# Optimization experiments

Hardware: AMD Instinct MI355X
Metric: run time of the kernel (lower is better)

The kernel has to match this reference:

```python
import jax, jax.numpy as jnp
import numpy as np

VOCAB, D = 100000, 128
B, V, S = 1024, 20, 30
N_CLASS = 20
H0, H1 = 256, 128  # hidden_dims


def setup_inputs() -> dict:
    key = jax.random.key(0)
    ks = jax.random.split(key, 10)
    diag_idx = jax.random.randint(ks[0], (B, V, S), 0, VOCAB, dtype=jnp.int32)
    proc_idx = jax.random.randint(ks[1], (B, V, S), 0, VOCAB, dtype=jnp.int32)
    embedding = jax.random.normal(ks[2], (VOCAB, D), dtype=jnp.float32)
    # fc0: (2D -> H0), fc1: (H0 -> H1), fc2: (H1 -> n_class); torch Linear layout [out,in]
    W0 = jax.random.normal(ks[3], (H0, 2 * D), dtype=jnp.float32) * (1.0 / np.sqrt(2 * D))
    b0 = jnp.zeros((H0,), dtype=jnp.float32)
    W1 = jax.random.normal(ks[4], (H1, H0), dtype=jnp.float32) * (1.0 / np.sqrt(H0))
    b1 = jnp.zeros((H1,), dtype=jnp.float32)
    W2 = jax.random.normal(ks[5], (N_CLASS, H1), dtype=jnp.float32) * (1.0 / np.sqrt(H1))
    b2 = jnp.zeros((N_CLASS,), dtype=jnp.float32)
    return {"diag_idx": diag_idx, "proc_idx": proc_idx, "embedding": embedding,
            "W0": W0, "b0": b0, "W1": W1, "b1": b1, "W2": W2, "b2": b2}


def _pool(embedding, idx):
    # gather [B,V,S,D], mean over set dim S, sum over visit dim V -> [B,D]
    e = embedding[idx]
    return e.mean(axis=2).sum(axis=1)


def reference(diag_idx, proc_idx, embedding, W0, b0, W1, b1, W2, b2):
    d = _pool(embedding, diag_idx)            # [B, D]
    p = _pool(embedding, proc_idx)            # [B, D]
    x = jnp.concatenate([d, p], axis=-1)      # [B, 2D]
    out = x @ W0.T + b0                        # fc_layers[0]
    out = jax.nn.relu(out) @ W1.T + b1         # relu applied before each subsequent layer
    out = jax.nn.relu(out) @ W2.T + b2
    return out                                  # [B, n_class]
```

## Files before the change

kernel.cpp:

```cpp
#include <hip/hip_runtime.h>

#define BATCH 1024
#define VS 600
#define D 128
#define H0 256
#define H1 128
#define NCLASS 20
#define CAP 128


__global__ __launch_bounds__(256) void bucket_kernel(
    const int* __restrict__ diag_idx, const int* __restrict__ proc_idx,
    unsigned short* __restrict__ lists, int* __restrict__ counts)
{
    __shared__ int cnt[16];
    const int s = blockIdx.x, tid = threadIdx.x;
    if (tid < 16) cnt[tid] = 0;
    __syncthreads();

    const int* dsrc = diag_idx + s * VS;
    const int* psrc = proc_idx + s * VS;
    for (int i = tid; i < VS; i += 256) {
        const int r = dsrc[i];
        const int b = r & 7;
        const int pos = atomicAdd(&cnt[b], 1);
        if (pos < CAP) lists[(s * 16 + b) * CAP + pos] = (unsigned short)(r >> 3);
        const int r2 = psrc[i];
        const int b2 = 8 + (r2 & 7);
        const int pos2 = atomicAdd(&cnt[b2], 1);
        if (pos2 < CAP) lists[(s * 16 + b2) * CAP + pos2] = (unsigned short)(r2 >> 3);
    }
    __syncthreads();
    if (tid < 16) counts[s * 16 + tid] = min(cnt[tid], CAP);
}

__global__ __launch_bounds__(256) void gather_partial_kernel(
    const unsigned short* __restrict__ lists, const int* __restrict__ counts,
    const float* __restrict__ emb, float* __restrict__ part)
{
    __shared__ unsigned short lq[2 * CAP];
    __shared__ int c2[2];
    __shared__ __attribute__((aligned(16))) float red[8][D];

    const int bid = blockIdx.x;
    const int x   = bid & 7;
    const int s   = bid >> 3;
    const int tid = threadIdx.x;

    if (tid < 2) c2[tid] = counts[s * 16 + tid * 8 + x];
    if (tid < CAP)           lq[tid] = lists[(s * 16 + x) * CAP + tid];
    else if (tid < 2 * CAP)  lq[tid] = lists[(s * 16 + 8 + x) * CAP + (tid - CAP)];
    __syncthreads();

    const int grp = tid >> 5, lane = tid & 31;
    const int pool = grp >> 2, sub = grp & 3;
    const int cnt = c2[pool];
    const unsigned short* lp = lq + pool * CAP;
    float4 acc = make_float4(0.f, 0.f, 0.f, 0.f);
    #pragma unroll 4
    for (int i = sub; i < cnt; i += 4) {
        const int row = ((int)lp[i] << 3) | x;
        const float4 e = ((const float4*)(emb + row * D))[lane];
        acc.x += e.x; acc.y += e.y; acc.z += e.z; acc.w += e.w;
    }
    ((float4*)red[grp])[lane] = acc;
    __syncthreads();

    {
        const int p = tid >> 7, d = tid & 127;
        const float v = red[p*4+0][d] + red[p*4+1][d] + red[p*4+2][d] + red[p*4+3][d];
        part[(x * BATCH + s) * (2 * D) + tid] = v * (1.0f / 30.0f);
    }
}

__global__ __launch_bounds__(256) void mlp_kernel(
    const float* __restrict__ part,
    const float* __restrict__ W0, const float* __restrict__ b0,
    const float* __restrict__ W1, const float* __restrict__ b1,
    const float* __restrict__ W2, const float* __restrict__ b2,
    float* __restrict__ out)
{
    __shared__ __attribute__((aligned(16))) float xs [8][2 * D];
    __shared__ __attribute__((aligned(16))) float h0s[8][H0];
    __shared__ __attribute__((aligned(16))) float h1s[8][H1];

    const int s0 = blockIdx.x * 8, tid = threadIdx.x;

    #pragma unroll
    for (int j = 0; j < 8; ++j) {
        float v = 0.f;
        #pragma unroll
        for (int xp = 0; xp < 8; ++xp)
            v += part[(xp * BATCH + s0 + j) * (2 * D) + tid];
        xs[j][tid] = v;
    }
    __syncthreads();

    {
        const float4* wrow = (const float4*)(W0 + tid * (2 * D));
        float a[8];
        #pragma unroll
        for (int j = 0; j < 8; ++j) a[j] = b0[tid];
        for (int k = 0; k < 64; ++k) {
            const float4 w = wrow[k];
            #pragma unroll
            for (int j = 0; j < 8; ++j) {
                const float4 xx = ((const float4*)xs[j])[k];
                a[j] += w.x * xx.x + w.y * xx.y + w.z * xx.z + w.w * xx.w;
            }
        }
        #pragma unroll
        for (int j = 0; j < 8; ++j) h0s[j][tid] = fmaxf(a[j], 0.f);
    }
    __syncthreads();

    if (tid < H1) {
        const float4* wrow = (const float4*)(W1 + tid * H0);
        float a[8];
        #pragma unroll
        for (int j = 0; j < 8; ++j) a[j] = b1[tid];
        for (int k = 0; k < 64; ++k) {
            const float4 w = wrow[k];
            #pragma unroll
            for (int j = 0; j < 8; ++j) {
                const float4 hh = ((const float4*)h0s[j])[k];
                a[j] += w.x * hh.x + w.y * hh.y + w.z * hh.z + w.w * hh.w;
            }
        }
        #pragma unroll
        for (int j = 0; j < 8; ++j) h1s[j][tid] = fmaxf(a[j], 0.f);
    }
    __syncthreads();

    if (tid < 8 * NCLASS) {
        const int row = tid >> 3, j = tid & 7;
        const float4* wrow = (const float4*)(W2 + row * H1);
        float a = b2[row];
        for (int k = 0; k < 32; ++k) {
            const float4 w = wrow[k];
            const float4 hh = ((const float4*)h1s[j])[k];
            a += w.x * hh.x + w.y * hh.y + w.z * hh.z + w.w * hh.w;
        }
        out[(s0 + j) * NCLASS + row] = a;
    }
}

extern "C" void kernel_launch(void* const* d_in, const int* in_sizes, int n_in,
                              void* d_out, int out_size, void* d_ws, size_t ws_size,
                              hipStream_t stream) {
    const int*   diag_idx = (const int*)d_in[0];
    const int*   proc_idx = (const int*)d_in[1];
    const float* emb      = (const float*)d_in[2];
    const float* W0       = (const float*)d_in[3];
    const float* b0       = (const float*)d_in[4];
    const float* W1       = (const float*)d_in[5];
    const float* b1       = (const float*)d_in[6];
    const float* W2       = (const float*)d_in[7];
    const float* b2       = (const float*)d_in[8];
    float* out = (float*)d_out;

    char* ws = (char*)d_ws;
    float*          part   = (float*)ws;
    unsigned short* lists  = (unsigned short*)(ws + 8*1024*1024);
    int*            counts = (int*)(ws + 12*1024*1024);

    bucket_kernel<<<BATCH, 256, 0, stream>>>(diag_idx, proc_idx, lists, counts);
    gather_partial_kernel<<<8 * BATCH, 256, 0, stream>>>(lists, counts, emb, part);
    mlp_kernel<<<BATCH / 8, 256, 0, stream>>>(part, W0, b0, W1, b1, W2, b2, out);
}
```

Measured before the change: 186.3 us.

## Repartition MLP kernel: fewer samples per block, split-K across lanes with shuffles

Restructures the MLP kernel so each block handles 4 samples instead of 8 and uses 512 threads. Each layer's dot products are split across 2 or 4 lanes along K and combined with xor shuffles. The goal is more blocks (256 instead of 128) to fill the GPU and to keep all threads busy in layers 1 and 2, where many used to sit idle. In exchange, W0 and W1 are re-read from global/L2 by twice as many blocks, and shuffle reductions add overhead.

```diff
diff --git a/kernel.cpp b/kernel.cpp
--- a/kernel.cpp
+++ b/kernel.cpp
@@ -7,6 +7,7 @@
 #define H1 128
 #define NCLASS 20
 #define CAP 128
+#define SPB 4
 
 
 __global__ __launch_bounds__(256) void bucket_kernel(
@@ -73,75 +74,92 @@
     }
 }
 
-__global__ __launch_bounds__(256) void mlp_kernel(
+__global__ __launch_bounds__(512) void mlp_kernel(
     const float* __restrict__ part,
     const float* __restrict__ W0, const float* __restrict__ b0,
     const float* __restrict__ W1, const float* __restrict__ b1,
     const float* __restrict__ W2, const float* __restrict__ b2,
     float* __restrict__ out)
 {
-    __shared__ __attribute__((aligned(16))) float xs [8][2 * D];
-    __shared__ __attribute__((aligned(16))) float h0s[8][H0];
-    __shared__ __attribute__((aligned(16))) float h1s[8][H1];
+    __shared__ __attribute__((aligned(16))) float xs [SPB][2 * D];
+    __shared__ __attribute__((aligned(16))) float h0s[SPB][H0];
+    __shared__ __attribute__((aligned(16))) float h1s[SPB][H1];
 
-    const int s0 = blockIdx.x * 8, tid = threadIdx.x;
+    const int s0 = blockIdx.x * SPB, tid = threadIdx.x;
 
     #pragma unroll
-    for (int j = 0; j < 8; ++j) {
+    for (int t = tid; t < SPB * 2 * D; t += 512) {
+        const int j = t >> 8, d = t & 255;
         float v = 0.f;
         #pragma unroll
         for (int xp = 0; xp < 8; ++xp)
-            v += part[(xp * BATCH + s0 + j) * (2 * D) + tid];
-        xs[j][tid] = v;
+            v += part[(xp * BATCH + s0 + j) * (2 * D) + d];
+        xs[j][d] = v;
     }
     __syncthreads();
 
     {
-        const float4* wrow = (const float4*)(W0 + tid * (2 * D));
-        float a[8];
+        const int row = tid >> 1, half = tid & 1;
+        const float4* wrow = (const float4*)(W0 + row * (2 * D) + half * D);
+        const int xoff = half * (D / 4);
+        float a[SPB];
         #pragma unroll
-        for (int j = 0; j < 8; ++j) a[j] = b0[tid];
-        for (int k = 0; k < 64; ++k) {
+        for (int j = 0; j < SPB; ++j) a[j] = 0.f;
+        #pragma unroll 4
+        for (int k = 0; k < 32; ++k) {
             const float4 w = wrow[k];
             #pragma unroll
-            for (int j = 0; j < 8; ++j) {
-                const float4 xx = ((const float4*)xs[j])[k];
+            for (int j = 0; j < SPB; ++j) {
+                const float4 xx = ((const float4*)xs[j])[xoff + k];
                 a[j] += w.x * xx.x + w.y * xx.y + w.z * xx.z + w.w * xx.w;
             }
         }
         #pragma unroll
-        for (int j = 0; j < 8; ++j) h0s[j][tid] = fmaxf(a[j], 0.f);
+        for (int j = 0; j < SPB; ++j) {
+            a[j] += __shfl_xor(a[j], 1);
+            if (!half) h0s[j][row] = fmaxf(a[j] + b0[row], 0.f);
+        }
     }
     __syncthreads();
 
-    if (tid < H1) {
-        const float4* wrow = (const float4*)(W1 + tid * H0);
-        float a[8];
+    {
+        const int row = tid >> 2, q = tid & 3;
+        const float4* wrow = (const float4*)(W1 + row * H0 + q * 64);
+        const int hoff = q * 16;
+        float a[SPB];
         #pragma unroll
-        for (int j = 0; j < 8; ++j) a[j] = b1[tid];
-        for (int k = 0; k < 64; ++k) {
+        for (int j = 0; j < SPB; ++j) a[j] = 0.f;
+        #pragma unroll 4
+        for (int k = 0; k < 16; ++k) {
             const float4 w = wrow[k];
             #pragma unroll
-            for (int j = 0; j < 8; ++j) {
-                const float4 hh = ((const float4*)h0s[j])[k];
+            for (int j = 0; j < SPB; ++j) {
+                const float4 hh = ((const float4*)h0s[j])[hoff + k];
                 a[j] += w.x * hh.x + w.y * hh.y + w.z * hh.z + w.w * hh.w;
             }
         }
         #pragma unroll
-        for (int j = 0; j < 8; ++j) h1s[j][tid] = fmaxf(a[j], 0.f);
+        for (int j = 0; j < SPB; ++j) {
+            a[j] += __shfl_xor(a[j], 1);
+            a[j] += __shfl_xor(a[j], 2);
+            if (!q) h1s[j][row] = fmaxf(a[j] + b1[row], 0.f);
+        }
     }
     __syncthreads();
 
-    if (tid < 8 * NCLASS) {
-        const int row = tid >> 3, j = tid & 7;
-        const float4* wrow = (const float4*)(W2 + row * H1);
-        float a = b2[row];
-        for (int k = 0; k < 32; ++k) {
-            const float4 w = wrow[k];
-            const float4 hh = ((const float4*)h1s[j])[k];
+    if (tid < NCLASS * 16) {
+        const int row = tid >> 4, q = (tid >> 2) & 3, j = tid & 3;
+        const float4* wrow = (const float4*)(W2 + row * H1 + q * 32);
+        const float4* hv   = (const float4*)(h1s[j] + q * 32);
+        float a = 0.f;
+        #pragma unroll
+        for (int k = 0; k < 8; ++k) {
+            const float4 w = wrow[k], hh = hv[k];
             a += w.x * hh.x + w.y * hh.y + w.z * hh.z + w.w * hh.w;
         }
-        out[(s0 + j) * NCLASS + row] = a;
+        a += __shfl_xor(a, 4);
+        a += __shfl_xor(a, 8);
+        if (!q) out[(s0 + j) * NCLASS + row] = a + b2[row];
     }
 }
 
@@ -166,5 +184,5 @@
 
     bucket_kernel<<<BATCH, 256, 0, stream>>>(diag_idx, proc_idx, lists, counts);
     gather_partial_kernel<<<8 * BATCH, 256, 0, stream>>>(lists, counts, emb, part);
-    mlp_kernel<<<BATCH / 8, 256, 0, stream>>>(part, W0, b0, W1, b1, W2, b2, out);
+    mlp_kernel<<<BATCH / SPB, 512, 0, stream>>>(part, W0, b0, W1, b1, W2, b2, out);
 }
```

Result: faster. 153.9 us (-17.4%).
